# Performance work log

Hardware: AMD Instinct MI355X
Metric: run time of the kernel (lower is better)

The kernel has to match this reference:

```python
import jax, jax.numpy as jnp
import numpy as np

K = 3          # kernel_size
DEG_P = 6      # numerator coeffs (order 5)
DEG_Q = 4      # denominator coeffs (powers 1..4)


def setup_inputs() -> dict:
    key = jax.random.key(0)
    k1, k2, k3 = jax.random.split(key, 3)
    B, Cin, Cout, H, W = 4, 16, 16, 64, 64
    x = jax.random.normal(k1, (B, Cin, H, W), dtype=jnp.float32)
    # per (out_channel f, in_channel c, kernel position p) rational coefficients
    A = jax.random.normal(k2, (Cout, Cin, K * K, DEG_P), dtype=jnp.float32) * 0.1
    Bc = jax.random.normal(k3, (Cout, Cin, K * K, DEG_Q), dtype=jnp.float32) * 0.1
    return {"x": x, "A": A, "Bc": Bc}


def reference(x, A, Bc):
    # x: [B, C, H, W]; A: [F, C, K*K, 6]; Bc: [F, C, K*K, 4]
    B, C, H, W = x.shape
    pad = (K - 1) // 2
    xp = jnp.pad(x, ((0, 0), (0, 0), (pad, pad), (pad, pad)))
    # sliding windows, one slice per kernel offset -> [K*K, B, C, H, W]
    wins = jnp.stack([xp[:, :, i:i + H, j:j + W]
                      for i in range(K) for j in range(K)])
    # powers x^0..x^5 -> [K*K, B, C, H, W, 6]
    pw = wins[..., None] ** jnp.arange(DEG_P, dtype=x.dtype)
    P = jnp.einsum('pbchwi,fcpi->fpbchw', pw, A)
    Q = 1.0 + jnp.abs(jnp.einsum('pbchwi,fcpi->fpbchw', pw[..., 1:1 + DEG_Q], Bc))
    # sum over kernel positions (p) and input channels (c) -> [F, B, H, W]
    out = jnp.sum(P / Q, axis=(1, 3))
    return jnp.transpose(out, (1, 0, 2, 3))  # [B, F, H, W]
```

## Files before the change

kernel.cpp:

```cpp
#include <hip/hip_runtime.h>


#define BB   4
#define CIN  16
#define COUT 16
#define HH   64
#define WW   64

__global__ __launch_bounds__(1024, 4) void KAConv_kernel(
    const float* __restrict__ x,
    const float* __restrict__ A,
    const float* __restrict__ Bc,
    float* __restrict__ out)
{
    const int blk = blockIdx.x;
    const int row = blk & 63;
    const int b   = blk >> 6;

    const int tid = threadIdx.x;
    const int c   = __builtin_amdgcn_readfirstlane(tid >> 6);
    const int w   = tid & 63;

    __shared__ float sRed[CIN][COUT][WW];

    const float* __restrict__ xc = x + (b * CIN + c) * (HH * WW);
    float win[3][3];
    #pragma unroll
    for (int i = 0; i < 3; ++i) {
        const int hh   = row - 1 + i;
        const bool okh = (hh >= 0) & (hh < HH);
        #pragma unroll
        for (int j = 0; j < 3; ++j) {
            const int wj  = w - 1 + j;
            const bool ok = okh & (wj >= 0) & (wj < WW);
            win[i][j] = ok ? xc[hh * WW + wj] : 0.0f;
        }
    }

    #pragma unroll 1
    for (int f = 0; f < COUT; ++f) {
        const float* __restrict__ Ac = A  + (f * CIN + c) * 54;
        const float* __restrict__ Bq = Bc + (f * CIN + c) * 36;

        float facc = 0.0f;
        #pragma unroll
        for (int p = 0; p < 9; ++p) {
            const float v = win[p / 3][p % 3];
            const float a0 = Ac[p*6+0], a1 = Ac[p*6+1], a2 = Ac[p*6+2];
            const float a3 = Ac[p*6+3], a4 = Ac[p*6+4], a5 = Ac[p*6+5];
            const float b1 = Bq[p*4+0], b2 = Bq[p*4+1];
            const float b3 = Bq[p*4+2], b4 = Bq[p*4+3];

            float P = a5;
            P = fmaf(P, v, a4); P = fmaf(P, v, a3); P = fmaf(P, v, a2);
            P = fmaf(P, v, a1); P = fmaf(P, v, a0);

            float q = b4;
            q = fmaf(q, v, b3); q = fmaf(q, v, b2); q = fmaf(q, v, b1);
            q *= v;

            const float d = 1.0f + fabsf(q);
            facc = fmaf(P, __builtin_amdgcn_rcpf(d), facc);
        }
        sRed[c][f][w] = facc;
    }
    __syncthreads();

    {
        const int f  = tid >> 6;
        const int px = tid & 63;
        float s = 0.0f;
        #pragma unroll
        for (int k = 0; k < CIN; ++k) s += sRed[k][f][px];
        out[((b * COUT + f) * HH + row) * WW + px] = s;
    }
}

extern "C" void kernel_launch(void* const* d_in, const int* in_sizes, int n_in,
                              void* d_out, int out_size, void* d_ws, size_t ws_size,
                              hipStream_t stream) {
    const float* x  = (const float*)d_in[0];
    const float* A  = (const float*)d_in[1];
    const float* Bc = (const float*)d_in[2];
    float* out = (float*)d_out;

    const int grid = BB * HH;
    KAConv_kernel<<<grid, 1024, 0, stream>>>(x, A, Bc, out);
}
```

Before: 23.41 us.

## Remap threads to output channels with per-thread pixel strips and repacked weights

Adds a repack kernel that reorders A and Bc so coefficients for consecutive output channels sit contiguously per (c, p), allowing vectorized loads. The main kernel now assigns lanes to output channels, with each thread computing 8 adjacent pixels over 2 input channels. Input windows are staged in shared memory, the grid is split into half-rows, and the shared-memory reduction is smaller. This removes the serial per-f loop with wave-uniform scalar coefficient loads and reuses each coefficient load across 8 pixels, at the cost of an extra kernel launch and more register pressure.

```diff
diff --git a/kernel.cpp b/kernel.cpp
--- a/kernel.cpp
+++ b/kernel.cpp
@@ -1,78 +1,134 @@
 #include <hip/hip_runtime.h>
 
 
-#define BB   4
 #define CIN  16
 #define COUT 16
 #define HH   64
 #define WW   64
 
-__global__ __launch_bounds__(1024, 4) void KAConv_kernel(
-    const float* __restrict__ x,
+typedef float f2 __attribute__((ext_vector_type(2)));
+typedef float f4 __attribute__((ext_vector_type(4)));
+
+#define NA (CIN * 9 * COUT * 6)
+#define NB (CIN * 9 * COUT * 4)
+
+__global__ __launch_bounds__(256) void repack_kernel(
     const float* __restrict__ A,
     const float* __restrict__ Bc,
+    float* __restrict__ ws)
+{
+    const int i = blockIdx.x * 256 + threadIdx.x;
+    if (i < NA) {
+        const int i6 = i % 6;  const int r  = i / 6;
+        const int f  = r & 15; const int r2 = r >> 4;
+        const int p  = r2 % 9; const int c  = r2 / 9;
+        ws[i] = A[((f * 16 + c) * 9 + p) * 6 + i6];
+    } else if (i < NA + NB) {
+        const int j  = i - NA;
+        const int i4 = j & 3;  const int r  = j >> 2;
+        const int f  = r & 15; const int r2 = r >> 4;
+        const int p  = r2 % 9; const int c  = r2 / 9;
+        ws[i] = Bc[((f * 16 + c) * 9 + p) * 4 + i4];
+    }
+}
+
+__global__ __launch_bounds__(512, 4) void KAConv_kernel(
+    const float* __restrict__ x,
+    const float* __restrict__ cw,
     float* __restrict__ out)
 {
-    const int blk = blockIdx.x;
-    const int row = blk & 63;
-    const int b   = blk >> 6;
+    const int blk  = blockIdx.x;
+    const int half = blk & 1;
+    const int row  = (blk >> 1) & 63;
+    const int b    = blk >> 7;
+    const int cb   = half << 5;
 
-    const int tid = threadIdx.x;
-    const int c   = __builtin_amdgcn_readfirstlane(tid >> 6);
-    const int w   = tid & 63;
+    const int tid  = threadIdx.x;
+    const int team = tid >> 6;
+    const int lane = tid & 63;
+    const int f    = lane & 15;
+    const int slot = lane >> 4;
 
-    __shared__ float sRed[CIN][COUT][WW];
+    const float* __restrict__ cA = cw;
+    const float* __restrict__ cB = cw + NA;
 
-    const float* __restrict__ xc = x + (b * CIN + c) * (HH * WW);
-    float win[3][3];
+    __shared__ float winS[CIN][3][36];
+    __shared__ float sRed[8][COUT][33];
+
+    for (int i = tid; i < CIN * 3 * 36; i += 512) {
+        const int c   = i / 108;
+        const int rem = i - c * 108;
+        const int ri  = rem / 36;
+        const int tc  = rem - ri * 36;
+        const int gh  = row - 1 + ri;
+        const int gw  = cb - 1 + tc;
+        const bool ok = (tc < 34) & (gh >= 0) & (gh < HH) & (gw >= 0) & (gw < WW);
+        winS[c][ri][tc] = ok ? x[((b * CIN + c) * HH + gh) * WW + gw] : 0.0f;
+    }
+    __syncthreads();
+
+    float acc[8];
     #pragma unroll
-    for (int i = 0; i < 3; ++i) {
-        const int hh   = row - 1 + i;
-        const bool okh = (hh >= 0) & (hh < HH);
+    for (int q = 0; q < 8; ++q) acc[q] = 0.0f;
+
+    const int fA = f * 6;
+    const int fB = f * 4;
+
+    #pragma unroll
+    for (int c2 = 0; c2 < 2; ++c2) {
+        const int c = team * 2 + c2;
+
+        float wr[3][10];
         #pragma unroll
-        for (int j = 0; j < 3; ++j) {
-            const int wj  = w - 1 + j;
-            const bool ok = okh & (wj >= 0) & (wj < WW);
-            win[i][j] = ok ? xc[hh * WW + wj] : 0.0f;
+        for (int ri = 0; ri < 3; ++ri) {
+            const float* wsrc = &winS[c][ri][slot * 8];
+            const f4 w0 = *(const f4*)(wsrc);
+            const f4 w1 = *(const f4*)(wsrc + 4);
+            const f2 w2 = *(const f2*)(wsrc + 8);
+            wr[ri][0] = w0.x; wr[ri][1] = w0.y; wr[ri][2] = w0.z; wr[ri][3] = w0.w;
+            wr[ri][4] = w1.x; wr[ri][5] = w1.y; wr[ri][6] = w1.z; wr[ri][7] = w1.w;
+            wr[ri][8] = w2.x; wr[ri][9] = w2.y;
+        }
+
+        #pragma unroll
+        for (int p = 0; p < 9; ++p) {
+            const int ri = p / 3, j = p % 3;
+            const float* pA = cA + (c * 9 + p) * 96 + fA;
+            const float* pB = cB + (c * 9 + p) * 64 + fB;
+            const f2 a01 = *(const f2*)(pA);
+            const f2 a23 = *(const f2*)(pA + 2);
+            const f2 a45 = *(const f2*)(pA + 4);
+            const f4 b14 = *(const f4*)(pB);
+
+            #pragma unroll
+            for (int qi = 0; qi < 8; ++qi) {
+                const float v = wr[ri][qi + j];
+                float P = a45.y;
+                P = fmaf(P, v, a45.x); P = fmaf(P, v, a23.y);
+                P = fmaf(P, v, a23.x); P = fmaf(P, v, a01.y);
+                P = fmaf(P, v, a01.x);
+                float q = b14.w;
+                q = fmaf(q, v, b14.z); q = fmaf(q, v, b14.y);
+                q = fmaf(q, v, b14.x);
+                q *= v;
+                const float d = 1.0f + fabsf(q);
+                acc[qi] = fmaf(P, __builtin_amdgcn_rcpf(d), acc[qi]);
+            }
         }
     }
 
-    #pragma unroll 1
-    for (int f = 0; f < COUT; ++f) {
-        const float* __restrict__ Ac = A  + (f * CIN + c) * 54;
-        const float* __restrict__ Bq = Bc + (f * CIN + c) * 36;
-
-        float facc = 0.0f;
-        #pragma unroll
-        for (int p = 0; p < 9; ++p) {
-            const float v = win[p / 3][p % 3];
-            const float a0 = Ac[p*6+0], a1 = Ac[p*6+1], a2 = Ac[p*6+2];
-            const float a3 = Ac[p*6+3], a4 = Ac[p*6+4], a5 = Ac[p*6+5];
-            const float b1 = Bq[p*4+0], b2 = Bq[p*4+1];
-            const float b3 = Bq[p*4+2], b4 = Bq[p*4+3];
-
-            float P = a5;
-            P = fmaf(P, v, a4); P = fmaf(P, v, a3); P = fmaf(P, v, a2);
-            P = fmaf(P, v, a1); P = fmaf(P, v, a0);
-
-            float q = b4;
-            q = fmaf(q, v, b3); q = fmaf(q, v, b2); q = fmaf(q, v, b1);
-            q *= v;
-
-            const float d = 1.0f + fabsf(q);
-            facc = fmaf(P, __builtin_amdgcn_rcpf(d), facc);
-        }
-        sRed[c][f][w] = facc;
-    }
+    #pragma unroll
+    for (int qi = 0; qi < 8; ++qi)
+        sRed[team][f][slot * 8 + qi] = acc[qi];
     __syncthreads();
 
     {
-        const int f  = tid >> 6;
-        const int px = tid & 63;
+        const int fo = tid >> 5;
+        const int px = tid & 31;
         float s = 0.0f;
         #pragma unroll
-        for (int k = 0; k < CIN; ++k) s += sRed[k][f][px];
-        out[((b * COUT + f) * HH + row) * WW + px] = s;
+        for (int k = 0; k < 8; ++k) s += sRed[k][fo][px];
+        out[((b * COUT + fo) * HH + row) * WW + cb + px] = s;
     }
 }
 
@@ -83,7 +139,11 @@
     const float* A  = (const float*)d_in[1];
     const float* Bc = (const float*)d_in[2];
     float* out = (float*)d_out;
+    float* cw  = (float*)d_ws;
 
-    const int grid = BB * HH;
-    KAConv_kernel<<<grid, 1024, 0, stream>>>(x, A, Bc, out);
+    const int nrep = NA + NB;
+    repack_kernel<<<(nrep + 255) / 256, 256, 0, stream>>>(A, Bc, cw);
+
+    const int grid = 4 * HH * 2;
+    KAConv_kernel<<<grid, 512, 0, stream>>>(x, cw, out);
 }
```

After: 48.75 us. 108% more time.

## Tile blocks over output channel and 8-row groups, reusing coefficients across rows

Applied to the files above, without the earlier changes.

The work split moves from one block per (batch, row) covering all 16 output channels to one block per (batch, output channel, 8-row group). Each thread loads a 10x3 input window once and applies one set of rational coefficients across 8 output rows. This replaces the per-f coefficient loads with per-row reuse and raises the grid from 256 to 512 blocks for better CU fill. In exchange, halo rows are reloaded across blocks and each block recomputes its input windows for every output channel, so register pressure rises and the launch bound is tightened to 8 waves per EU.

```diff
diff --git a/kernel.cpp b/kernel.cpp
--- a/kernel.cpp
+++ b/kernel.cpp
@@ -7,72 +7,78 @@
 #define HH   64
 #define WW   64
 
-__global__ __launch_bounds__(1024, 4) void KAConv_kernel(
+__global__ __launch_bounds__(1024, 8) void KAConv_kernel(
     const float* __restrict__ x,
     const float* __restrict__ A,
     const float* __restrict__ Bc,
     float* __restrict__ out)
 {
     const int blk = blockIdx.x;
-    const int row = blk & 63;
-    const int b   = blk >> 6;
+    const int rg  = blk & 7;
+    const int f   = (blk >> 3) & 15;
+    const int b   = blk >> 7;
 
-    const int tid = threadIdx.x;
-    const int c   = __builtin_amdgcn_readfirstlane(tid >> 6);
-    const int w   = tid & 63;
+    const int tid   = threadIdx.x;
+    const int c     = __builtin_amdgcn_readfirstlane(tid >> 6);
+    const int w     = tid & 63;
+    const int rbase = rg << 3;
 
-    __shared__ float sRed[CIN][COUT][WW];
+    const float* __restrict__ xc = x  + (b * CIN + c) * (HH * WW);
+    const float* __restrict__ Ac = A  + (f * CIN + c) * 54;
+    const float* __restrict__ Bq = Bc + (f * CIN + c) * 36;
 
-    const float* __restrict__ xc = x + (b * CIN + c) * (HH * WW);
-    float win[3][3];
+    float win[10][3];
     #pragma unroll
-    for (int i = 0; i < 3; ++i) {
-        const int hh   = row - 1 + i;
+    for (int rr = 0; rr < 10; ++rr) {
+        const int hh   = rbase - 1 + rr;
         const bool okh = (hh >= 0) & (hh < HH);
         #pragma unroll
         for (int j = 0; j < 3; ++j) {
             const int wj  = w - 1 + j;
             const bool ok = okh & (wj >= 0) & (wj < WW);
-            win[i][j] = ok ? xc[hh * WW + wj] : 0.0f;
+            win[rr][j] = ok ? xc[hh * WW + wj] : 0.0f;
         }
     }
 
-    #pragma unroll 1
-    for (int f = 0; f < COUT; ++f) {
-        const float* __restrict__ Ac = A  + (f * CIN + c) * 54;
-        const float* __restrict__ Bq = Bc + (f * CIN + c) * 36;
+    float acc[8];
+    #pragma unroll
+    for (int r = 0; r < 8; ++r) acc[r] = 0.0f;
 
-        float facc = 0.0f;
+    #pragma unroll
+    for (int p = 0; p < 9; ++p) {
+        const int pi = p / 3, pj = p % 3;
+        const float a0 = Ac[p*6+0], a1 = Ac[p*6+1], a2 = Ac[p*6+2];
+        const float a3 = Ac[p*6+3], a4 = Ac[p*6+4], a5 = Ac[p*6+5];
+        const float b1 = Bq[p*4+0], b2 = Bq[p*4+1];
+        const float b3 = Bq[p*4+2], b4 = Bq[p*4+3];
+
         #pragma unroll
-        for (int p = 0; p < 9; ++p) {
-            const float v = win[p / 3][p % 3];
-            const float a0 = Ac[p*6+0], a1 = Ac[p*6+1], a2 = Ac[p*6+2];
-            const float a3 = Ac[p*6+3], a4 = Ac[p*6+4], a5 = Ac[p*6+5];
-            const float b1 = Bq[p*4+0], b2 = Bq[p*4+1];
-            const float b3 = Bq[p*4+2], b4 = Bq[p*4+3];
-
+        for (int r = 0; r < 8; ++r) {
+            const float v = win[r + pi][pj];
             float P = a5;
             P = fmaf(P, v, a4); P = fmaf(P, v, a3); P = fmaf(P, v, a2);
             P = fmaf(P, v, a1); P = fmaf(P, v, a0);
-
             float q = b4;
             q = fmaf(q, v, b3); q = fmaf(q, v, b2); q = fmaf(q, v, b1);
             q *= v;
+            const float d = 1.0f + fabsf(q);
+            acc[r] = fmaf(P, __builtin_amdgcn_rcpf(d), acc[r]);
+        }
+    }
 
-            const float d = 1.0f + fabsf(q);
-            facc = fmaf(P, __builtin_amdgcn_rcpf(d), facc);
-        }
-        sRed[c][f][w] = facc;
-    }
+    __shared__ float sRed[CIN][8][66];
+    #pragma unroll
+    for (int r = 0; r < 8; ++r)
+        sRed[c][r][w] = acc[r];
     __syncthreads();
 
-    {
-        const int f  = tid >> 6;
-        const int px = tid & 63;
+    if (tid < 512) {
+        const int row = tid >> 6;
+        const int px  = tid & 63;
         float s = 0.0f;
         #pragma unroll
-        for (int k = 0; k < CIN; ++k) s += sRed[k][f][px];
-        out[((b * COUT + f) * HH + row) * WW + px] = s;
+        for (int k = 0; k < CIN; ++k) s += sRed[k][row][px];
+        out[((b * COUT + f) * HH + rbase + row) * WW + px] = s;
     }
 }
 
@@ -84,6 +90,6 @@
     const float* Bc = (const float*)d_in[2];
     float* out = (float*)d_out;
 
-    const int grid = BB * HH;
+    const int grid = BB * COUT * (HH / 8);
     KAConv_kernel<<<grid, 1024, 0, stream>>>(x, A, Bc, out);
 }
```

Result: faster. 20.10 us (-14.1%).

## Remap blocks to (batch, output channel, row group) with rolling row window

Applied to the files above, without the earlier changes.

Each block now handles one output channel and 16 rows instead of one row and all 16 output channels. Each thread's coefficients are fixed for the whole block, so they can stay in registers, and a rolling 3-row window reuses input loads across rows. The grid size is unchanged, but the compute per thread is identical. This mainly removes per-f coefficient reloads, in exchange for more register pressure from holding 90 coefficients.

```diff
diff --git a/kernel.cpp b/kernel.cpp
--- a/kernel.cpp
+++ b/kernel.cpp
@@ -7,6 +7,15 @@
 #define HH   64
 #define WW   64
 
+static __device__ __forceinline__ void loadrow(const float* __restrict__ xc,
+                                               int hh, int w, float u[3]) {
+    const bool okh = (hh >= 0) & (hh < HH);
+    const float* __restrict__ rw = xc + hh * WW;
+    u[0] = (okh & (w >= 1))      ? rw[w - 1] : 0.0f;
+    u[1] = okh                   ? rw[w]     : 0.0f;
+    u[2] = (okh & (w <= WW - 2)) ? rw[w + 1] : 0.0f;
+}
+
 __global__ __launch_bounds__(1024, 4) void KAConv_kernel(
     const float* __restrict__ x,
     const float* __restrict__ A,
@@ -14,65 +23,62 @@
     float* __restrict__ out)
 {
     const int blk = blockIdx.x;
-    const int row = blk & 63;
+    const int f   = blk & 15;
+    const int rg  = (blk >> 4) & 3;
     const int b   = blk >> 6;
 
-    const int tid = threadIdx.x;
-    const int c   = __builtin_amdgcn_readfirstlane(tid >> 6);
-    const int w   = tid & 63;
+    const int tid   = threadIdx.x;
+    const int c     = __builtin_amdgcn_readfirstlane(tid >> 6);
+    const int w     = tid & 63;
+    const int rbase = rg << 4;
 
-    __shared__ float sRed[CIN][COUT][WW];
+    const float* __restrict__ xc = x  + (b * CIN + c) * (HH * WW);
+    const float* __restrict__ Ac = A  + (f * CIN + c) * 54;
+    const float* __restrict__ Bq = Bc + (f * CIN + c) * 36;
 
-    const float* __restrict__ xc = x + (b * CIN + c) * (HH * WW);
-    float win[3][3];
-    #pragma unroll
-    for (int i = 0; i < 3; ++i) {
-        const int hh   = row - 1 + i;
-        const bool okh = (hh >= 0) & (hh < HH);
+    __shared__ float sRed[CIN][16][64];
+
+    float u0[3], u1[3], u2[3];
+    loadrow(xc, rbase - 1, w, u0);
+    loadrow(xc, rbase,     w, u1);
+    loadrow(xc, rbase + 1, w, u2);
+
+#define TAP(p, v) {                                                         \
+        float P = Ac[(p)*6+5];                                              \
+        P = fmaf(P, (v), Ac[(p)*6+4]); P = fmaf(P, (v), Ac[(p)*6+3]);       \
+        P = fmaf(P, (v), Ac[(p)*6+2]); P = fmaf(P, (v), Ac[(p)*6+1]);       \
+        P = fmaf(P, (v), Ac[(p)*6+0]);                                      \
+        float q = Bq[(p)*4+3];                                              \
+        q = fmaf(q, (v), Bq[(p)*4+2]); q = fmaf(q, (v), Bq[(p)*4+1]);       \
+        q = fmaf(q, (v), Bq[(p)*4+0]); q *= (v);                            \
+        acc[(p)/3] = fmaf(P, __builtin_amdgcn_rcpf(1.0f + fabsf(q)),        \
+                          acc[(p)/3]); }
+
+    #pragma unroll 4
+    for (int r = 0; r < 16; ++r) {
+        float un[3];
+        loadrow(xc, rbase + r + 2, w, un);
+
+        float acc[3] = {0.0f, 0.0f, 0.0f};
+        TAP(0, u0[0]) TAP(1, u0[1]) TAP(2, u0[2])
+        TAP(3, u1[0]) TAP(4, u1[1]) TAP(5, u1[2])
+        TAP(6, u2[0]) TAP(7, u2[1]) TAP(8, u2[2])
+        sRed[c][r][w] = (acc[0] + acc[1]) + acc[2];
+
         #pragma unroll
-        for (int j = 0; j < 3; ++j) {
-            const int wj  = w - 1 + j;
-            const bool ok = okh & (wj >= 0) & (wj < WW);
-            win[i][j] = ok ? xc[hh * WW + wj] : 0.0f;
-        }
+        for (int j = 0; j < 3; ++j) { u0[j] = u1[j]; u1[j] = u2[j]; u2[j] = un[j]; }
     }
+#undef TAP
 
-    #pragma unroll 1
-    for (int f = 0; f < COUT; ++f) {
-        const float* __restrict__ Ac = A  + (f * CIN + c) * 54;
-        const float* __restrict__ Bq = Bc + (f * CIN + c) * 36;
-
-        float facc = 0.0f;
-        #pragma unroll
-        for (int p = 0; p < 9; ++p) {
-            const float v = win[p / 3][p % 3];
-            const float a0 = Ac[p*6+0], a1 = Ac[p*6+1], a2 = Ac[p*6+2];
-            const float a3 = Ac[p*6+3], a4 = Ac[p*6+4], a5 = Ac[p*6+5];
-            const float b1 = Bq[p*4+0], b2 = Bq[p*4+1];
-            const float b3 = Bq[p*4+2], b4 = Bq[p*4+3];
-
-            float P = a5;
-            P = fmaf(P, v, a4); P = fmaf(P, v, a3); P = fmaf(P, v, a2);
-            P = fmaf(P, v, a1); P = fmaf(P, v, a0);
-
-            float q = b4;
-            q = fmaf(q, v, b3); q = fmaf(q, v, b2); q = fmaf(q, v, b1);
-            q *= v;
-
-            const float d = 1.0f + fabsf(q);
-            facc = fmaf(P, __builtin_amdgcn_rcpf(d), facc);
-        }
-        sRed[c][f][w] = facc;
-    }
     __syncthreads();
 
     {
-        const int f  = tid >> 6;
-        const int px = tid & 63;
+        const int row = tid >> 6;
+        const int col = tid & 63;
         float s = 0.0f;
         #pragma unroll
-        for (int k = 0; k < CIN; ++k) s += sRed[k][f][px];
-        out[((b * COUT + f) * HH + row) * WW + px] = s;
+        for (int k = 0; k < CIN; ++k) s += sRed[k][row][col];
+        out[((b * COUT + f) * HH + rbase + row) * WW + col] = s;
     }
 }
 
@@ -84,6 +90,6 @@
     const float* Bc = (const float*)d_in[2];
     float* out = (float*)d_out;
 
-    const int grid = BB * HH;
+    const int grid = BB * 4 * COUT;
     KAConv_kernel<<<grid, 1024, 0, stream>>>(x, A, Bc, out);
 }
```

Result: faster. 19.39 us (-17.2%).
